# Optimization experiments

Measured on AMD Instinct MI355X. Metric: run time of the kernel, lower is better.

Reference implementation:

```python
import jax, jax.numpy as jnp
import numpy as np

NB = 5  # frequency bands


def _ln(x, g, b, eps=1e-5):
    m = jnp.mean(x, axis=-1, keepdims=True)
    v = jnp.var(x, axis=-1, keepdims=True)
    return (x - m) / jnp.sqrt(v + eps) * g + b


def _graph_adj(x, adj_w, sw1, sb1, sw2, sb2, pos_factor, pos_enc):
    # x: [B, D, N] -> degree-normalized adjacency [B, N, N]
    d = x.shape[1]
    xt = jnp.swapaxes(x, 1, 2)  # [B, N, D]
    # concat-MLP first layer split: cat(xi, xj) @ W1 == xi @ W1[:d] + xj @ W1[d:]
    a = xt @ sw1[:d]
    bpart = xt @ sw1[d:]
    h = jax.nn.elu(a[:, :, None, :] + bpart[:, None, :, :] + sb1)  # [B, N, N, H]
    dyn = jax.nn.sigmoid(jnp.squeeze(h @ sw2, -1) + sb2)  # [B, N, N]
    static = jax.nn.softmax(adj_w, axis=-1)
    pos = jax.nn.softmax(pos_enc, axis=-1)
    comb = jax.nn.softmax(static + dyn + pos_factor * pos, axis=-1)
    deg = jnp.sum(comb, axis=-1)
    dis = (deg + 1e-8) ** -0.5
    return dis[:, :, None] * comb * dis[:, None, :]


def _gcn(x, adj, w, b):
    # x: [B, D, N], adj: [B, N, N] -> [B, D_out, N]
    xt = jnp.swapaxes(x, 1, 2)
    out = jnp.einsum('bij,bjd->bid', adj, xt) @ w + b
    return jnp.swapaxes(out, 1, 2)


def _mha(x, qkv_w, qkv_b, ow, ob, nh=4):
    B, S, D = x.shape
    dh = D // nh
    q, k, v = jnp.split(x @ qkv_w + qkv_b, 3, axis=-1)
    q = q.reshape(B, S, nh, dh)
    k = k.reshape(B, S, nh, dh)
    v = v.reshape(B, S, nh, dh)
    att = jax.nn.softmax(jnp.einsum('bihd,bjhd->bhij', q, k) / float(np.sqrt(dh)), axis=-1)
    o = jnp.einsum('bhij,bjhd->bihd', att, v).reshape(B, S, D)
    return o @ ow + ob


def setup_inputs():
    key = jax.random.key(0)
    B, D, N = 16, 256, 64
    ks = iter(jax.random.split(key, 40))

    def rn(shape, s=0.05):
        return jax.random.normal(next(ks), shape, dtype=jnp.float32) * s

    eyeN = jnp.eye(N, dtype=jnp.float32)
    return dict(
        feature=jax.random.normal(next(ks), (B, NB * D, 1, N), dtype=jnp.float32),
        l_adj_w=jnp.tile(eyeN[None], (NB, 1, 1)),
        l_sim_w1=rn((NB, 2 * D, D)), l_sim_b1=jnp.zeros((NB, D), jnp.float32),
        l_sim_w2=rn((NB, D, 1)), l_sim_b2=jnp.zeros((NB, 1), jnp.float32),
        l_pos_factor=jnp.full((NB,), 0.5, jnp.float32),
        l_pos_enc=jnp.tile(eyeN[None], (NB, 1, 1)),
        l_gcn_w=rn((NB, D, D)), l_gcn_b=jnp.zeros((NB, D), jnp.float32),
        g_adj_w=jnp.eye(NB, dtype=jnp.float32),
        g_sim_w1=rn((2 * D, D)), g_sim_b1=jnp.zeros((D,), jnp.float32),
        g_sim_w2=rn((D, 1)), g_sim_b2=jnp.zeros((1,), jnp.float32),
        g_pos_factor=jnp.float32(0.5),
        g_pos_enc=jnp.eye(NB, dtype=jnp.float32),
        g_gcn_w=rn((D, D)), g_gcn_b=jnp.zeros((D,), jnp.float32),
        qkv_w=rn((D, 3 * D)), qkv_b=jnp.zeros((3 * D,), jnp.float32),
        attn_ow=rn((D, D)), attn_ob=jnp.zeros((D,), jnp.float32),
        ln1_g=jnp.ones((D,), jnp.float32), ln1_b=jnp.zeros((D,), jnp.float32),
        ln2_g=jnp.ones((D,), jnp.float32), ln2_b=jnp.zeros((D,), jnp.float32),
        mlp_w1=rn((D, 4 * D)), mlp_b1=jnp.zeros((4 * D,), jnp.float32),
        mlp_w2=rn((4 * D, D)), mlp_b2=jnp.zeros((D,), jnp.float32),
        imp_w=rn((NB, N, 1)), imp_b=jnp.zeros((NB, 1), jnp.float32),
    )


def reference(feature, l_adj_w, l_sim_w1, l_sim_b1, l_sim_w2, l_sim_b2,
              l_pos_factor, l_pos_enc, l_gcn_w, l_gcn_b,
              g_adj_w, g_sim_w1, g_sim_b1, g_sim_w2, g_sim_b2,
              g_pos_factor, g_pos_enc, g_gcn_w, g_gcn_b,
              qkv_w, qkv_b, attn_ow, attn_ob,
              ln1_g, ln1_b, ln2_g, ln2_b,
              mlp_w1, mlp_b1, mlp_w2, mlp_b2,
              imp_w, imp_b):
    B = feature.shape[0]
    D = l_gcn_w.shape[-1]
    N = feature.shape[-1]
    # [B, 5*D, 1, N] -> [5, B, D, N] band-major
    x5 = jnp.moveaxis(feature.reshape(B, NB, D, N), 1, 0)
    # per-band local graphs + GCNs (vmapped over the 5 bands)
    local_adj = jax.vmap(_graph_adj)(x5, l_adj_w, l_sim_w1, l_sim_b1,
                                     l_sim_w2, l_sim_b2, l_pos_factor, l_pos_enc)
    local_out = jax.vmap(_gcn)(x5, local_adj, l_gcn_w, l_gcn_b)  # [5, B, D, N]
    scale_nodes = jnp.moveaxis(jnp.mean(local_out, axis=-1), 0, 1)  # [B, 5, D]
    # cross-band attention block (pre: MHA + residual + LN, then MLP + residual + LN)
    attn = _mha(scale_nodes, qkv_w, qkv_b, attn_ow, attn_ob)
    h1 = _ln(scale_nodes + attn, ln1_g, ln1_b)
    mlp = jax.nn.gelu(h1 @ mlp_w1 + mlp_b1, approximate=False) @ mlp_w2 + mlp_b2
    se = _ln(h1 + mlp, ln2_g, ln2_b)  # [B, 5, D]
    # global scale graph over the 5 band nodes
    xg = jnp.swapaxes(se, 1, 2)  # [B, D, 5]
    g_adj = _graph_adj(xg, g_adj_w, g_sim_w1, g_sim_b1, g_sim_w2, g_sim_b2,
                       g_pos_factor, g_pos_enc)
    g_out = jnp.swapaxes(_gcn(xg, g_adj, g_gcn_w, g_gcn_b), 1, 2)  # [B, 5, D]
    # modulate each local band feature by its global scale vector
    enh = local_out * jnp.moveaxis(g_out, 1, 0)[..., None]  # [5, B, D, N]
    # per-band importance projection over channels: [5, B, D, 1]
    out5 = jnp.einsum('kbdn,kno->kbdo', enh, imp_w) + imp_b[:, None, None, :]
    output = jnp.moveaxis(out5, 0, 1).reshape(B, NB * D, 1, 1)
    return output, g_adj, jnp.moveaxis(local_out, 0, 1)
```

## Files before the change

kernel.cpp:

```cpp
#include <hip/hip_runtime.h>
#include <hip/hip_bf16.h>

#define NBANDS 5
#define BATCH  16
#define DIM    256
#define NNODE  64
#define SEQ    5
#define NHEAD  4
#define DHEAD  64

typedef __hip_bfloat16 bf16;
typedef unsigned short ushort_t;
typedef __attribute__((ext_vector_type(8))) short short8;
typedef __attribute__((ext_vector_type(4))) float float4v;

__device__ __forceinline__ float bu2f(ushort_t u){
    bf16 h = *reinterpret_cast<bf16*>(&u);
    return __bfloat162float(h);
}
__device__ __forceinline__ ushort_t f2bu(float x){
    bf16 h = __float2bfloat16(x);
    return *reinterpret_cast<ushort_t*>(&h);
}

__global__ void __launch_bounds__(256) k_head(
    const float* __restrict__ l_adj_w, const float* __restrict__ l_pos_enc,
    const float* __restrict__ l_pf,
    const float* __restrict__ g_adj_w, const float* __restrict__ g_pos_enc,
    const float* __restrict__ g_pf,
    float* __restrict__ sbase, float* __restrict__ gbase,
    const float* __restrict__ w1, const float* __restrict__ gw,
    ushort_t* __restrict__ w1bt, ushort_t* __restrict__ gwbt,
    const float* __restrict__ feat,
    ushort_t* __restrict__ xtb, ushort_t* __restrict__ xtT)
{
    int blk = blockIdx.x;
    int tid = threadIdx.x;
    __shared__ ushort_t tile[64][65];

    if (blk < 80) {
        int r = blk*4 + (tid>>6);
        int k = r >> 6, i = r & 63;
        int t = tid & 63;
        float aw = l_adj_w[(k*NNODE + i)*NNODE + t];
        float pe = l_pos_enc[(k*NNODE + i)*NNODE + t];
        float m1 = aw, m2 = pe;
        for (int o=32;o>0;o>>=1){ m1 = fmaxf(m1, __shfl_xor(m1,o,64)); m2 = fmaxf(m2, __shfl_xor(m2,o,64)); }
        float e1 = __expf(aw-m1), e2 = __expf(pe-m2);
        float s1=e1, s2=e2;
        for (int o=32;o>0;o>>=1){ s1 += __shfl_xor(s1,o,64); s2 += __shfl_xor(s2,o,64); }
        float pf = l_pf[k];
        sbase[(k*NNODE+i)*NNODE + t] = e1/s1 + pf*(e2/s2);
    } else if (blk == 80) {
        if (tid < NBANDS) {
            int i = tid;
            float r1[NBANDS], r2[NBANDS];
            float m1=-1e30f, m2=-1e30f;
            for (int j=0;j<NBANDS;j++){
                r1[j]=g_adj_w[i*NBANDS+j]; r2[j]=g_pos_enc[i*NBANDS+j];
                m1=fmaxf(m1,r1[j]); m2=fmaxf(m2,r2[j]);
            }
            float s1=0.f,s2=0.f;
            for (int j=0;j<NBANDS;j++){ r1[j]=__expf(r1[j]-m1); r2[j]=__expf(r2[j]-m2); s1+=r1[j]; s2+=r2[j]; }
            float pf = g_pf[0];
            for (int j=0;j<NBANDS;j++) gbase[i*NBANDS+j] = r1[j]/s1 + pf*(r2[j]/s2);
        }
    } else if (blk < 321) {
        int idx = blk - 81;
        int inst = idx >> 4;
        int t = idx & 15;
        int r0 = (t>>2)*64, c0 = (t&3)*64;
        const float* src; ushort_t* dst;
        if (inst < 10){
            int k = inst>>1, half = inst&1;
            src = w1  + ((size_t)k*512 + half*256)*256;
            dst = w1bt+ ((size_t)k*512 + half*256)*256;
        } else {
            int k = inst-10;
            src = gw  + (size_t)k*65536;
            dst = gwbt+ (size_t)k*65536;
        }
        int jj = tid & 63, i4 = tid >> 6;
        for (int p=0;p<16;p++){
            int i = p*4 + i4;
            tile[i][jj] = f2bu(src[(size_t)(r0+i)*256 + c0 + jj]);
        }
        __syncthreads();
        for (int p=0;p<16;p++){
            int i = p*4 + i4;
            dst[(size_t)(c0+i)*256 + r0 + jj] = tile[jj][i];
        }
    } else {
        int idx = blk - 321;
        int k = idx >> 6;
        int b = (idx >> 2) & 15;
        int dt = idx & 3;
        const float* src = feat + ((size_t)b*NBANDS*DIM + (size_t)k*DIM)*NNODE;
        ushort_t* dst = xtb + (size_t)(k*BATCH+b)*NNODE*DIM;
        ushort_t* dstT = xtT + (size_t)(k*BATCH+b)*DIM*NNODE;
        for (int u=0; u<16; ++u){
            int i = dt*4096 + u*256 + tid;
            dstT[i] = f2bu(src[i]);
        }
        for (int r=0;r<16;r++){
            int dp = r*4 + (tid>>6);
            int n  = tid & 63;
            tile[dp][n] = f2bu(src[(size_t)(dt*64+dp)*NNODE + n]);
        }
        __syncthreads();
        for (int r=0;r<16;r++){
            int n  = r*4 + (tid>>6);
            int dp = tid & 63;
            dst[(size_t)n*DIM + dt*64 + dp] = tile[dp][n];
        }
    }
}

__global__ void __launch_bounds__(256) k_ab_mfma(const ushort_t* __restrict__ xtb,
                        const ushort_t* __restrict__ w1bt, const float* __restrict__ b1,
                        ushort_t* __restrict__ aab, ushort_t* __restrict__ bbb)
{
    int blk = blockIdx.x;
    int kband = blk / (BATCH*8);
    int b = (blk/8) % BATCH;
    int nblk = blk & 7;
    int tid = threadIdx.x;
    int wave = tid>>6, lane = tid&63;
    int c16 = lane & 15, quad = lane >> 4;
    int m0 = wave*16;
    size_t rowbase = (size_t)(kband*BATCH+b)*NNODE;
    const ushort_t* Aptr = xtb + (rowbase + m0 + c16)*DIM + quad*8;
    const ushort_t* Bbase = w1bt + (size_t)kband*512*DIM;
    int ncol0 = nblk*64;
    const ushort_t* Bptr0 = Bbase + (size_t)(ncol0 +  0 + c16)*DIM + quad*8;
    const ushort_t* Bptr1 = Bbase + (size_t)(ncol0 + 16 + c16)*DIM + quad*8;
    const ushort_t* Bptr2 = Bbase + (size_t)(ncol0 + 32 + c16)*DIM + quad*8;
    const ushort_t* Bptr3 = Bbase + (size_t)(ncol0 + 48 + c16)*DIM + quad*8;
    float4v acc0 = {0.f,0.f,0.f,0.f}, acc1 = acc0, acc2 = acc0, acc3 = acc0;
    #pragma unroll
    for (int ks=0; ks<8; ++ks){
        short8 a  = *reinterpret_cast<const short8*>(Aptr  + ks*32);
        short8 b0 = *reinterpret_cast<const short8*>(Bptr0 + ks*32);
        short8 b1v= *reinterpret_cast<const short8*>(Bptr1 + ks*32);
        short8 b2 = *reinterpret_cast<const short8*>(Bptr2 + ks*32);
        short8 b3 = *reinterpret_cast<const short8*>(Bptr3 + ks*32);
        acc0 = __builtin_amdgcn_mfma_f32_16x16x32_bf16(a, b0, acc0, 0,0,0);
        acc1 = __builtin_amdgcn_mfma_f32_16x16x32_bf16(a, b1v, acc1, 0,0,0);
        acc2 = __builtin_amdgcn_mfma_f32_16x16x32_bf16(a, b2, acc2, 0,0,0);
        acc3 = __builtin_amdgcn_mfma_f32_16x16x32_bf16(a, b3, acc3, 0,0,0);
    }
    int half = nblk >> 2;
    int cbase = (nblk & 3)*64;
    ushort_t* dst = half ? bbb : aab;
    float4v accs[4] = {acc0, acc1, acc2, acc3};
    #pragma unroll
    for (int nt=0; nt<4; ++nt){
        int cg = cbase + nt*16 + c16;
        float bias = half ? 0.f : b1[kband*DIM + cg];
        #pragma unroll
        for (int r=0;r<4;r++){
            int m = m0 + quad*4 + r;
            dst[(rowbase + m)*DIM + cg] = f2bu(accs[nt][r] + bias);
        }
    }
}

__global__ void __launch_bounds__(256) k_dyn_comb(const ushort_t* __restrict__ aab,
                           const ushort_t* __restrict__ bbb,
                           const float* __restrict__ w2, const float* __restrict__ b2arr,
                           const float* __restrict__ sbase,
                           ushort_t* __restrict__ combb)
{
    int blk = blockIdx.x;
    int k = blk / (BATCH*16);
    int b = (blk / 16) % BATCH;
    int i0 = (blk % 16) * 4;
    int kb = k*BATCH + b;
    __shared__ ushort_t bs[64][260];
    __shared__ float arows[4][DIM];
    __shared__ float w2s[DIM];
    int tid = threadIdx.x;
    int wave = tid >> 6, lane = tid & 63;
    const ushort_t* bsrc = bbb + (size_t)kb*NNODE*DIM;
    for (int u=0; u<16; ++u){
        int idx = u*1024 + tid*4;
        int row = idx >> 8, col = idx & 255;
        *reinterpret_cast<ushort4*>(&bs[row][col]) =
            *reinterpret_cast<const ushort4*>(&bsrc[(size_t)row*DIM + col]);
    }
    for (int r=0;r<4;r++) arows[r][tid] = bu2f(aab[((size_t)kb*NNODE + i0 + r)*DIM + tid]);
    w2s[tid] = w2[k*DIM + tid];
    __syncthreads();

    int i = i0 + wave;
    float acc = 0.f;
    #pragma unroll 4
    for (int dd=0; dd<64; ++dd){
        ushort4 bv = *reinterpret_cast<const ushort4*>(&bs[lane][dd*4]);
        float4 av = *reinterpret_cast<const float4*>(&arows[wave][dd*4]);
        float4 wv = *reinterpret_cast<const float4*>(&w2s[dd*4]);
        float v0 = av.x + bu2f(bv.x);
        float v1 = av.y + bu2f(bv.y);
        float v2 = av.z + bu2f(bv.z);
        float v3 = av.w + bu2f(bv.w);
        float e0 = (v0>0.f)? v0 : (__expf(v0)-1.f);
        float e1 = (v1>0.f)? v1 : (__expf(v1)-1.f);
        float e2 = (v2>0.f)? v2 : (__expf(v2)-1.f);
        float e3 = (v3>0.f)? v3 : (__expf(v3)-1.f);
        acc += e0*wv.x + e1*wv.y + e2*wv.z + e3*wv.w;
    }
    float sb2 = b2arr[k];
    float sg = 1.f/(1.f + __expf(-(acc + sb2)));
    float val = sbase[(k*NNODE + i)*NNODE + lane] + sg;
    float m = val;
    for (int o=32;o>0;o>>=1) m = fmaxf(m, __shfl_xor(m,o,64));
    float e = __expf(val - m);
    float s = e;
    for (int o=32;o>0;o>>=1) s += __shfl_xor(s,o,64);
    combb[((size_t)kb*NNODE + i)*NNODE + lane] = f2bu(e/s);
}

__global__ void __launch_bounds__(256) k_y_mfma(const ushort_t* __restrict__ combb,
                       const ushort_t* __restrict__ xtT,
                       ushort_t* __restrict__ yb)
{
    int blk = blockIdx.x;
    int kband = blk / (BATCH*4);
    int b = (blk/4) % BATCH;
    int nblk = blk & 3;
    int tid = threadIdx.x;
    int wave = tid>>6, lane = tid&63;
    int c16 = lane & 15, quad = lane >> 4;
    int m0 = wave*16;
    int kb = kband*BATCH + b;
    const ushort_t* Aptr = combb + ((size_t)kb*NNODE + m0 + c16)*NNODE + quad*8;
    const ushort_t* Bbase = xtT + (size_t)kb*DIM*NNODE;
    int ncol0 = nblk*64;
    const ushort_t* Bptr0 = Bbase + (size_t)(ncol0 +  0 + c16)*NNODE + quad*8;
    const ushort_t* Bptr1 = Bbase + (size_t)(ncol0 + 16 + c16)*NNODE + quad*8;
    const ushort_t* Bptr2 = Bbase + (size_t)(ncol0 + 32 + c16)*NNODE + quad*8;
    const ushort_t* Bptr3 = Bbase + (size_t)(ncol0 + 48 + c16)*NNODE + quad*8;
    float4v acc0 = {0.f,0.f,0.f,0.f}, acc1 = acc0, acc2 = acc0, acc3 = acc0;
    #pragma unroll
    for (int ks=0; ks<2; ++ks){
        short8 a  = *reinterpret_cast<const short8*>(Aptr  + ks*32);
        short8 b0 = *reinterpret_cast<const short8*>(Bptr0 + ks*32);
        short8 b1v= *reinterpret_cast<const short8*>(Bptr1 + ks*32);
        short8 b2 = *reinterpret_cast<const short8*>(Bptr2 + ks*32);
        short8 b3 = *reinterpret_cast<const short8*>(Bptr3 + ks*32);
        acc0 = __builtin_amdgcn_mfma_f32_16x16x32_bf16(a, b0, acc0, 0,0,0);
        acc1 = __builtin_amdgcn_mfma_f32_16x16x32_bf16(a, b1v, acc1, 0,0,0);
        acc2 = __builtin_amdgcn_mfma_f32_16x16x32_bf16(a, b2, acc2, 0,0,0);
        acc3 = __builtin_amdgcn_mfma_f32_16x16x32_bf16(a, b3, acc3, 0,0,0);
    }
    size_t rowbase = (size_t)kb*NNODE;
    float4v accs[4] = {acc0, acc1, acc2, acc3};
    #pragma unroll
    for (int nt=0; nt<4; ++nt){
        int cg = ncol0 + nt*16 + c16;
        #pragma unroll
        for (int r=0;r<4;r++){
            int m = m0 + quad*4 + r;
            yb[(rowbase + m)*DIM + cg] = f2bu(accs[nt][r]);
        }
    }
}

__global__ void __launch_bounds__(256) k_gcn_mfma(const ushort_t* __restrict__ yb,
                         const ushort_t* __restrict__ gwbt, const float* __restrict__ gb,
                         const float* __restrict__ imp_w,
                         float* __restrict__ out_local,
                         float* __restrict__ scalew, float* __restrict__ impw)
{
    int blk = blockIdx.x;
    int kband = blk / (BATCH*4);
    int b = (blk/4) % BATCH;
    int nblk = blk & 3;
    int tid = threadIdx.x;
    int wave = tid>>6, lane = tid&63;
    int c16 = lane & 15, quad = lane >> 4;
    int m0 = wave*16;
    int kb = kband*BATCH + b;
    __shared__ float iw_s[NNODE];
    __shared__ float sred[4][64];
    __shared__ float ired[4][64];
    if (tid < NNODE) iw_s[tid] = imp_w[kband*NNODE + tid];
    const ushort_t* Aptr = yb + ((size_t)kb*NNODE + m0 + c16)*DIM + quad*8;
    const ushort_t* Bbase = gwbt + (size_t)kband*DIM*DIM;
    int ncol0 = nblk*64;
    const ushort_t* Bptr0 = Bbase + (size_t)(ncol0 +  0 + c16)*DIM + quad*8;
    const ushort_t* Bptr1 = Bbase + (size_t)(ncol0 + 16 + c16)*DIM + quad*8;
    const ushort_t* Bptr2 = Bbase + (size_t)(ncol0 + 32 + c16)*DIM + quad*8;
    const ushort_t* Bptr3 = Bbase + (size_t)(ncol0 + 48 + c16)*DIM + quad*8;
    float4v acc0 = {0.f,0.f,0.f,0.f}, acc1 = acc0, acc2 = acc0, acc3 = acc0;
    #pragma unroll
    for (int ks=0; ks<8; ++ks){
        short8 a  = *reinterpret_cast<const short8*>(Aptr  + ks*32);
        short8 b0 = *reinterpret_cast<const short8*>(Bptr0 + ks*32);
        short8 b1v= *reinterpret_cast<const short8*>(Bptr1 + ks*32);
        short8 b2 = *reinterpret_cast<const short8*>(Bptr2 + ks*32);
        short8 b3 = *reinterpret_cast<const short8*>(Bptr3 + ks*32);
        acc0 = __builtin_amdgcn_mfma_f32_16x16x32_bf16(a, b0, acc0, 0,0,0);
        acc1 = __builtin_amdgcn_mfma_f32_16x16x32_bf16(a, b1v, acc1, 0,0,0);
        acc2 = __builtin_amdgcn_mfma_f32_16x16x32_bf16(a, b2, acc2, 0,0,0);
        acc3 = __builtin_amdgcn_mfma_f32_16x16x32_bf16(a, b3, acc3, 0,0,0);
    }
    __syncthreads();
    float4v accs[4] = {acc0, acc1, acc2, acc3};
    #pragma unroll
    for (int nt=0; nt<4; ++nt){
        int cg = ncol0 + nt*16 + c16;
        float bias = gb[kband*DIM + cg];
        float v0 = accs[nt][0]+bias, v1 = accs[nt][1]+bias, v2 = accs[nt][2]+bias, v3 = accs[nt][3]+bias;
        float4 v = make_float4(v0, v1, v2, v3);
        float* dst = out_local + ((size_t)(b*NBANDS + kband)*DIM + cg)*NNODE + m0 + quad*4;
        *reinterpret_cast<float4*>(dst) = v;
        int nb = m0 + quad*4;
        float s  = v0 + v1 + v2 + v3;
        float di = v0*iw_s[nb] + v1*iw_s[nb+1] + v2*iw_s[nb+2] + v3*iw_s[nb+3];
        s  += __shfl_xor(s, 16, 64);  s  += __shfl_xor(s, 32, 64);
        di += __shfl_xor(di, 16, 64); di += __shfl_xor(di, 32, 64);
        if (quad == 0){
            sred[wave][nt*16 + c16] = s;
            ired[wave][nt*16 + c16] = di;
        }
    }
    __syncthreads();
    if (tid < 64){
        float s  = sred[0][tid] + sred[1][tid] + sred[2][tid] + sred[3][tid];
        float di = ired[0][tid] + ired[1][tid] + ired[2][tid] + ired[3][tid];
        size_t o = ((size_t)b*SEQ + kband)*DIM + ncol0 + tid;
        scalew[o] = s * (1.f/64.f);
        impw[o]   = di;
    }
}

template<int COLS, int SLICES>
__global__ void __launch_bounds__(256) k_gemv(const float* __restrict__ x, const float* __restrict__ w,
                       const float* __restrict__ bias, float* __restrict__ out,
                       int K, int N, int act)
{
    int chunks = N / COLS;
    int row = blockIdx.x / chunks;
    int n0 = (blockIdx.x % chunks) * COLS;
    int c = threadIdx.x % COLS, s = threadIdx.x / COLS;
    __shared__ float xs[1024];
    __shared__ float part[SLICES][COLS];
    for (int i = threadIdx.x; i < K; i += 256) xs[i] = x[(size_t)row*K + i];
    __syncthreads();
    int klen = K / SLICES;
    const float* wp = w + (size_t)(s*klen)*N + n0 + c;
    const float* xp = xs + s*klen;
    float acc = 0.f;
    #pragma unroll 8
    for (int i = 0; i < klen; ++i) acc += xp[i] * wp[(size_t)i*N];
    part[s][c] = acc;
    __syncthreads();
    if (s == 0){
        float v = bias[n0+c];
        #pragma unroll
        for (int q=0;q<SLICES;q++) v += part[q][c];
        if (act) v = 0.5f*v*(1.f + erff(v*0.70710678118654752f));
        out[(size_t)row*N + n0 + c] = v;
    }
}

__global__ void __launch_bounds__(256) k_projattn(const float* __restrict__ qkvw,
                        const float* __restrict__ ow, const float* __restrict__ ob,
                        float* __restrict__ projw)
{
    int row = blockIdx.x / 4;
    int n0 = (blockIdx.x % 4) * 64;
    int b = row / SEQ, i = row % SEQ;
    int tid = threadIdx.x;
    int h = tid >> 6, l = tid & 63;
    __shared__ float xs[DIM];
    __shared__ float part[4][64];
    const float* base = qkvw + (size_t)b*SEQ*3*DIM;
    float qv = base[(size_t)i*3*DIM + h*DHEAD + l];
    float pj[SEQ];
    #pragma unroll
    for (int j=0;j<SEQ;j++){
        float p = qv * base[(size_t)j*3*DIM + DIM + h*DHEAD + l];
        for (int o=32;o>0;o>>=1) p += __shfl_xor(p,o,64);
        pj[j] = p * 0.125f;
    }
    float m = pj[0];
    #pragma unroll
    for (int j=1;j<SEQ;j++) m = fmaxf(m, pj[j]);
    float ssum = 0.f;
    #pragma unroll
    for (int j=0;j<SEQ;j++){ pj[j] = __expf(pj[j]-m); ssum += pj[j]; }
    float inv = 1.f/ssum;
    float o = 0.f;
    #pragma unroll
    for (int j=0;j<SEQ;j++) o += pj[j]*inv * base[(size_t)j*3*DIM + 2*DIM + h*DHEAD + l];
    xs[tid] = o;
    __syncthreads();
    int c = tid & 63, s = tid >> 6;
    const float* wp = ow + (size_t)(s*64)*DIM + n0 + c;
    const float* xp = xs + s*64;
    float acc = 0.f;
    #pragma unroll 8
    for (int k=0;k<64;++k) acc += xp[k] * wp[(size_t)k*DIM];
    part[s][c] = acc;
    __syncthreads();
    if (s == 0){
        projw[(size_t)row*DIM + n0 + c] = ob[n0+c] + part[0][c]+part[1][c]+part[2][c]+part[3][c];
    }
}

__device__ __forceinline__ float block_ln(float v, int tid, float* red, float g, float bln)
{
    float s = v;
    for (int o=32;o>0;o>>=1) s += __shfl_xor(s,o,64);
    int wave = tid>>6, lane = tid&63;
    if (lane==0) red[wave] = s;
    __syncthreads();
    float mean = (red[0]+red[1]+red[2]+red[3]) * (1.f/DIM);
    float c = v - mean;
    float q = c*c;
    for (int o=32;o>0;o>>=1) q += __shfl_xor(q,o,64);
    __syncthreads();
    if (lane==0) red[wave] = q;
    __syncthreads();
    float var = (red[0]+red[1]+red[2]+red[3]) * (1.f/DIM);
    return c * rsqrtf(var + 1e-5f) * g + bln;
}

__global__ void __launch_bounds__(256) k_mlp1_ln(const float* __restrict__ projw,
                         const float* __restrict__ scalew,
                         const float* __restrict__ ln1_g, const float* __restrict__ ln1_b,
                         const float* __restrict__ w1, const float* __restrict__ b1,
                         float* __restrict__ h1w, float* __restrict__ mhw)
{
    int row = blockIdx.x / 16;
    int n0 = (blockIdx.x % 16) * 64;
    int tid = threadIdx.x;
    __shared__ float xs[DIM];
    __shared__ float red[4];
    __shared__ float part[4][64];
    float v = projw[(size_t)row*DIM + tid] + scalew[(size_t)row*DIM + tid];
    float h = block_ln(v, tid, red, ln1_g[tid], ln1_b[tid]);
    xs[tid] = h;
    if ((blockIdx.x % 16) == 0) h1w[(size_t)row*DIM + tid] = h;
    __syncthreads();
    int c = tid & 63, s = tid >> 6;
    const float* wp = w1 + (size_t)(s*64)*1024 + n0 + c;
    const float* xp = xs + s*64;
    float acc = 0.f;
    #pragma unroll 8
    for (int i=0;i<64;++i) acc += xp[i] * wp[(size_t)i*1024];
    part[s][c] = acc;
    __syncthreads();
    if (s == 0){
        float o = b1[n0+c] + part[0][c] + part[1][c] + part[2][c] + part[3][c];
        o = 0.5f*o*(1.f + erff(o*0.70710678118654752f));
        mhw[(size_t)row*1024 + n0 + c] = o;
    }
}

__global__ void __launch_bounds__(256) k_gab_ln(const float* __restrict__ m2w,
                        const float* __restrict__ h1w,
                        const float* __restrict__ ln2_g, const float* __restrict__ ln2_b,
                        const float* __restrict__ gw1, const float* __restrict__ gb1,
                        float* __restrict__ sew, float* __restrict__ gaw, float* __restrict__ gbw)
{
    int row = blockIdx.x / 4;
    int n0 = (blockIdx.x % 4) * 64;
    int tid = threadIdx.x;
    __shared__ float xs[DIM];
    __shared__ float red[4];
    __shared__ float partA[4][64];
    __shared__ float partB[4][64];
    float v = m2w[(size_t)row*DIM + tid] + h1w[(size_t)row*DIM + tid];
    float h = block_ln(v, tid, red, ln2_g[tid], ln2_b[tid]);
    xs[tid] = h;
    if ((blockIdx.x % 4) == 0) sew[(size_t)row*DIM + tid] = h;
    __syncthreads();
    int c = tid & 63, s = tid >> 6;
    const float* wpA = gw1 + (size_t)(s*64)*DIM + n0 + c;
    const float* wpB = wpA + (size_t)DIM*DIM;
    const float* xp = xs + s*64;
    float aA = 0.f, aB = 0.f;
    #pragma unroll 8
    for (int i=0;i<64;++i){
        float xv = xp[i];
        aA += xv * wpA[(size_t)i*DIM];
        aB += xv * wpB[(size_t)i*DIM];
    }
    partA[s][c] = aA;
    partB[s][c] = aB;
    __syncthreads();
    if (s == 0){
        gaw[(size_t)row*DIM + n0 + c] = gb1[n0+c] + partA[0][c]+partA[1][c]+partA[2][c]+partA[3][c];
        gbw[(size_t)row*DIM + n0 + c] = partB[0][c]+partB[1][c]+partB[2][c]+partB[3][c];
    }
}

__global__ void __launch_bounds__(256) k_goutfin(const float* __restrict__ gaw,
                        const float* __restrict__ gbw,
                        const float* __restrict__ gw2, const float* __restrict__ gb2,
                        const float* __restrict__ gbase,
                        const float* __restrict__ sew,
                        const float* __restrict__ ggw, const float* __restrict__ ggb,
                        const float* __restrict__ impw, const float* __restrict__ imp_b,
                        float* __restrict__ out0, float* __restrict__ out_gadj)
{
    int row = blockIdx.x / 4;
    int n0 = (blockIdx.x % 4) * 64;
    int b = row / SEQ, i = row % SEQ;
    int tid = threadIdx.x;
    int wave = tid >> 6, lane = tid & 63;
    __shared__ float dyn_s[SEQ];
    __shared__ float xs[DIM];
    __shared__ float part[4][64];
    for (int j = wave; j < SEQ; j += 4){
        const float* gar = gaw + (size_t)row*DIM;
        const float* gbr = gbw + ((size_t)b*SEQ + j)*DIM;
        float acc = 0.f;
        #pragma unroll
        for (int m=0;m<4;m++){
            int dd = lane + m*64;
            float v = gar[dd] + gbr[dd];
            float e = (v>0.f) ? v : (__expf(v)-1.f);
            acc += e * gw2[dd];
        }
        for (int o=32;o>0;o>>=1) acc += __shfl_xor(acc,o,64);
        if (lane==0) dyn_s[j] = acc;
    }
    __syncthreads();
    float gc[SEQ];
    {
        float sb2 = gb2[0];
        float m = -1e30f;
        #pragma unroll
        for (int j=0;j<SEQ;j++){
            float sg = 1.f/(1.f+__expf(-(dyn_s[j]+sb2)));
            gc[j] = gbase[i*SEQ+j] + sg;
            m = fmaxf(m, gc[j]);
        }
        float ssum=0.f;
        #pragma unroll
        for (int j=0;j<SEQ;j++){ gc[j]=__expf(gc[j]-m); ssum+=gc[j]; }
        float inv = 1.f/ssum;
        #pragma unroll
        for (int j=0;j<SEQ;j++) gc[j] *= inv;
    }
    if (n0 == 0 && tid < SEQ) out_gadj[((size_t)b*SEQ+i)*SEQ + tid] = gc[tid];
    float t = 0.f;
    #pragma unroll
    for (int j=0;j<SEQ;j++) t += gc[j]*sew[((size_t)b*SEQ + j)*DIM + tid];
    xs[tid] = t;
    __syncthreads();
    int c = tid & 63, s = tid >> 6;
    const float* wp = ggw + (size_t)(s*64)*DIM + n0 + c;
    const float* xp = xs + s*64;
    float acc = 0.f;
    #pragma unroll 8
    for (int k=0;k<64;++k) acc += xp[k] * wp[(size_t)k*DIM];
    part[s][c] = acc;
    __syncthreads();
    if (s == 0){
        float g = ggb[n0+c] + part[0][c]+part[1][c]+part[2][c]+part[3][c];
        size_t o = (size_t)row*DIM + n0 + c;
        out0[o] = g * impw[o] + imp_b[i];
    }
}

extern "C" void kernel_launch(void* const* d_in, const int* in_sizes, int n_in,
                              void* d_out, int out_size, void* d_ws, size_t ws_size,
                              hipStream_t stream)
{
    const float* feature      = (const float*)d_in[0];
    const float* l_adj_w      = (const float*)d_in[1];
    const float* l_sim_w1     = (const float*)d_in[2];
    const float* l_sim_b1     = (const float*)d_in[3];
    const float* l_sim_w2     = (const float*)d_in[4];
    const float* l_sim_b2     = (const float*)d_in[5];
    const float* l_pos_factor = (const float*)d_in[6];
    const float* l_pos_enc    = (const float*)d_in[7];
    const float* l_gcn_w      = (const float*)d_in[8];
    const float* l_gcn_b      = (const float*)d_in[9];
    const float* g_adj_w      = (const float*)d_in[10];
    const float* g_sim_w1     = (const float*)d_in[11];
    const float* g_sim_b1     = (const float*)d_in[12];
    const float* g_sim_w2     = (const float*)d_in[13];
    const float* g_sim_b2     = (const float*)d_in[14];
    const float* g_pos_factor = (const float*)d_in[15];
    const float* g_pos_enc    = (const float*)d_in[16];
    const float* g_gcn_w      = (const float*)d_in[17];
    const float* g_gcn_b      = (const float*)d_in[18];
    const float* qkv_w        = (const float*)d_in[19];
    const float* qkv_b        = (const float*)d_in[20];
    const float* attn_ow      = (const float*)d_in[21];
    const float* attn_ob      = (const float*)d_in[22];
    const float* ln1_g        = (const float*)d_in[23];
    const float* ln1_b        = (const float*)d_in[24];
    const float* ln2_g        = (const float*)d_in[25];
    const float* ln2_b        = (const float*)d_in[26];
    const float* mlp_w1       = (const float*)d_in[27];
    const float* mlp_b1       = (const float*)d_in[28];
    const float* mlp_w2       = (const float*)d_in[29];
    const float* mlp_b2       = (const float*)d_in[30];
    const float* imp_w        = (const float*)d_in[31];
    const float* imp_b        = (const float*)d_in[32];

    float* out0      = (float*)d_out;
    float* out_gadj  = out0 + (size_t)BATCH*NBANDS*DIM;
    float* out_local = out_gadj + (size_t)BATCH*NBANDS*NBANDS;

    const size_t BIG = (size_t)NBANDS*BATCH*NNODE*DIM;
    ushort_t* xtb   = (ushort_t*)d_ws;
    ushort_t* aab   = xtb + BIG;
    ushort_t* bbb   = aab + BIG;
    ushort_t* xtT   = bbb + BIG;
    ushort_t* yb    = aab;
    ushort_t* w1bt  = xtT + BIG;
    ushort_t* gwbt  = w1bt + (size_t)NBANDS*512*DIM;
    ushort_t* combb = gwbt + (size_t)NBANDS*DIM*DIM;
    float* fp = (float*)(combb + (size_t)NBANDS*BATCH*NNODE*NNODE);
    float* sbase  = fp; fp += NBANDS*NNODE*NNODE;
    float* gbase  = fp; fp += 32;
    float* scalew = fp; fp += BATCH*SEQ*DIM;
    float* impw   = fp; fp += BATCH*SEQ*DIM;
    float* qkvw   = fp; fp += BATCH*SEQ*3*DIM;
    float* projw  = fp; fp += BATCH*SEQ*DIM;
    float* h1w    = fp; fp += BATCH*SEQ*DIM;
    float* mhw    = fp; fp += BATCH*SEQ*4*DIM;
    float* m2w    = fp; fp += BATCH*SEQ*DIM;
    float* sew    = fp; fp += BATCH*SEQ*DIM;
    float* gaw    = fp; fp += BATCH*SEQ*DIM;
    float* gbw    = fp; fp += BATCH*SEQ*DIM;

    const int ROWS = BATCH*SEQ;

    k_head<<<641, 256, 0, stream>>>(l_adj_w, l_pos_enc, l_pos_factor,
                                    g_adj_w, g_pos_enc, g_pos_factor,
                                    sbase, gbase,
                                    l_sim_w1, l_gcn_w, w1bt, gwbt,
                                    feature, xtb, xtT);
    k_ab_mfma<<<NBANDS*BATCH*8, 256, 0, stream>>>(xtb, w1bt, l_sim_b1, aab, bbb);
    k_dyn_comb<<<NBANDS*BATCH*16, 256, 0, stream>>>(aab, bbb, l_sim_w2, l_sim_b2, sbase, combb);
    k_y_mfma<<<NBANDS*BATCH*4, 256, 0, stream>>>(combb, xtT, yb);
    k_gcn_mfma<<<NBANDS*BATCH*4, 256, 0, stream>>>(yb, gwbt, l_gcn_b, imp_w,
                                                   out_local, scalew, impw);
    k_gemv<64,4><<<ROWS*12, 256, 0, stream>>>(scalew, qkv_w, qkv_b, qkvw, 256, 768, 0);
    k_projattn<<<ROWS*4, 256, 0, stream>>>(qkvw, attn_ow, attn_ob, projw);
    k_mlp1_ln<<<ROWS*16, 256, 0, stream>>>(projw, scalew, ln1_g, ln1_b, mlp_w1, mlp_b1, h1w, mhw);
    k_gemv<32,8><<<ROWS*8, 256, 0, stream>>>(mhw, mlp_w2, mlp_b2, m2w, 1024, 256, 0);
    k_gab_ln<<<ROWS*4, 256, 0, stream>>>(m2w, h1w, ln2_g, ln2_b, g_sim_w1, g_sim_b1, sew, gaw, gbw);
    k_goutfin<<<ROWS*4, 256, 0, stream>>>(gaw, gbw, g_sim_w2, g_sim_b2, gbase,
                                          sew, g_gcn_w, g_gcn_b, impw, imp_b,
                                          out0, out_gadj);
}
```

Measured before the change: 218.3 us.

## Fuse GCN tail with QKV projection and collapse attention/MLP chain into fewer kernels

Restructures the post-GCN pipeline so that one block per (band,batch) computes the full GCN output tile, reduces the node means, and immediately runs the QKV projection. Attention projection, residual and LN1 are then fused into one kernel, and both MLP layers, LN2 and the global-graph first layer into another. This removes several launches and intermediate buffers. In exchange it cuts parallelism sharply: 80 blocks instead of 320 or more per stage, and each thread walks long serial dot-product loops over the weights. Those long loops may become latency-bound on a GPU with many CUs.

```diff
diff --git a/kernel.cpp b/kernel.cpp
--- a/kernel.cpp
+++ b/kernel.cpp
@@ -266,148 +266,92 @@
     }
 }
 
-__global__ void __launch_bounds__(256) k_gcn_mfma(const ushort_t* __restrict__ yb,
-                         const ushort_t* __restrict__ gwbt, const float* __restrict__ gb,
-                         const float* __restrict__ imp_w,
-                         float* __restrict__ out_local,
-                         float* __restrict__ scalew, float* __restrict__ impw)
+__global__ void __launch_bounds__(256) k_gcn_qkv(const ushort_t* __restrict__ yb,
+                        const ushort_t* __restrict__ gwbt, const float* __restrict__ gb,
+                        const float* __restrict__ imp_w,
+                        const float* __restrict__ qkv_w, const float* __restrict__ qkv_b,
+                        float* __restrict__ out_local,
+                        float* __restrict__ scalew, float* __restrict__ impw,
+                        float* __restrict__ qkvw)
 {
     int blk = blockIdx.x;
-    int kband = blk / (BATCH*4);
-    int b = (blk/4) % BATCH;
-    int nblk = blk & 3;
+    int kband = blk / BATCH;
+    int b = blk % BATCH;
+    int kb = kband*BATCH + b;
     int tid = threadIdx.x;
     int wave = tid>>6, lane = tid&63;
     int c16 = lane & 15, quad = lane >> 4;
-    int m0 = wave*16;
-    int kb = kband*BATCH + b;
+    int ncol0 = wave*64;
     __shared__ float iw_s[NNODE];
-    __shared__ float sred[4][64];
-    __shared__ float ired[4][64];
+    __shared__ float s_lds[DIM];
     if (tid < NNODE) iw_s[tid] = imp_w[kband*NNODE + tid];
-    const ushort_t* Aptr = yb + ((size_t)kb*NNODE + m0 + c16)*DIM + quad*8;
+    __syncthreads();
+
     const ushort_t* Bbase = gwbt + (size_t)kband*DIM*DIM;
-    int ncol0 = nblk*64;
     const ushort_t* Bptr0 = Bbase + (size_t)(ncol0 +  0 + c16)*DIM + quad*8;
     const ushort_t* Bptr1 = Bbase + (size_t)(ncol0 + 16 + c16)*DIM + quad*8;
     const ushort_t* Bptr2 = Bbase + (size_t)(ncol0 + 32 + c16)*DIM + quad*8;
     const ushort_t* Bptr3 = Bbase + (size_t)(ncol0 + 48 + c16)*DIM + quad*8;
-    float4v acc0 = {0.f,0.f,0.f,0.f}, acc1 = acc0, acc2 = acc0, acc3 = acc0;
-    #pragma unroll
-    for (int ks=0; ks<8; ++ks){
-        short8 a  = *reinterpret_cast<const short8*>(Aptr  + ks*32);
-        short8 b0 = *reinterpret_cast<const short8*>(Bptr0 + ks*32);
-        short8 b1v= *reinterpret_cast<const short8*>(Bptr1 + ks*32);
-        short8 b2 = *reinterpret_cast<const short8*>(Bptr2 + ks*32);
-        short8 b3 = *reinterpret_cast<const short8*>(Bptr3 + ks*32);
-        acc0 = __builtin_amdgcn_mfma_f32_16x16x32_bf16(a, b0, acc0, 0,0,0);
-        acc1 = __builtin_amdgcn_mfma_f32_16x16x32_bf16(a, b1v, acc1, 0,0,0);
-        acc2 = __builtin_amdgcn_mfma_f32_16x16x32_bf16(a, b2, acc2, 0,0,0);
-        acc3 = __builtin_amdgcn_mfma_f32_16x16x32_bf16(a, b3, acc3, 0,0,0);
-    }
-    __syncthreads();
-    float4v accs[4] = {acc0, acc1, acc2, acc3};
+
+    float sacc[4] = {0.f,0.f,0.f,0.f};
+    float dacc[4] = {0.f,0.f,0.f,0.f};
+
+    for (int rt=0; rt<4; ++rt){
+        const ushort_t* Aptr = yb + ((size_t)kb*NNODE + rt*16 + c16)*DIM + quad*8;
+        float4v acc0 = {0.f,0.f,0.f,0.f}, acc1 = acc0, acc2 = acc0, acc3 = acc0;
+        #pragma unroll
+        for (int ks=0; ks<8; ++ks){
+            short8 a  = *reinterpret_cast<const short8*>(Aptr  + ks*32);
+            short8 b0 = *reinterpret_cast<const short8*>(Bptr0 + ks*32);
+            short8 b1v= *reinterpret_cast<const short8*>(Bptr1 + ks*32);
+            short8 b2 = *reinterpret_cast<const short8*>(Bptr2 + ks*32);
+            short8 b3 = *reinterpret_cast<const short8*>(Bptr3 + ks*32);
+            acc0 = __builtin_amdgcn_mfma_f32_16x16x32_bf16(a, b0, acc0, 0,0,0);
+            acc1 = __builtin_amdgcn_mfma_f32_16x16x32_bf16(a, b1v, acc1, 0,0,0);
+            acc2 = __builtin_amdgcn_mfma_f32_16x16x32_bf16(a, b2, acc2, 0,0,0);
+            acc3 = __builtin_amdgcn_mfma_f32_16x16x32_bf16(a, b3, acc3, 0,0,0);
+        }
+        float4v accs[4] = {acc0, acc1, acc2, acc3};
+        #pragma unroll
+        for (int nt=0; nt<4; ++nt){
+            int cg = ncol0 + nt*16 + c16;
+            float bias = gb[kband*DIM + cg];
+            float v0 = accs[nt][0]+bias, v1 = accs[nt][1]+bias,
+                  v2 = accs[nt][2]+bias, v3 = accs[nt][3]+bias;
+            float4 v = make_float4(v0, v1, v2, v3);
+            float* dst = out_local + ((size_t)(b*NBANDS + kband)*DIM + cg)*NNODE + rt*16 + quad*4;
+            *reinterpret_cast<float4*>(dst) = v;
+            int nb = rt*16 + quad*4;
+            sacc[nt] += v0 + v1 + v2 + v3;
+            dacc[nt] += v0*iw_s[nb] + v1*iw_s[nb+1] + v2*iw_s[nb+2] + v3*iw_s[nb+3];
+        }
+    }
+    size_t row = (size_t)b*SEQ + kband;
     #pragma unroll
     for (int nt=0; nt<4; ++nt){
-        int cg = ncol0 + nt*16 + c16;
-        float bias = gb[kband*DIM + cg];
-        float v0 = accs[nt][0]+bias, v1 = accs[nt][1]+bias, v2 = accs[nt][2]+bias, v3 = accs[nt][3]+bias;
-        float4 v = make_float4(v0, v1, v2, v3);
-        float* dst = out_local + ((size_t)(b*NBANDS + kband)*DIM + cg)*NNODE + m0 + quad*4;
-        *reinterpret_cast<float4*>(dst) = v;
-        int nb = m0 + quad*4;
-        float s  = v0 + v1 + v2 + v3;
-        float di = v0*iw_s[nb] + v1*iw_s[nb+1] + v2*iw_s[nb+2] + v3*iw_s[nb+3];
-        s  += __shfl_xor(s, 16, 64);  s  += __shfl_xor(s, 32, 64);
-        di += __shfl_xor(di, 16, 64); di += __shfl_xor(di, 32, 64);
+        float s = sacc[nt], d = dacc[nt];
+        s += __shfl_xor(s, 16, 64);  s += __shfl_xor(s, 32, 64);
+        d += __shfl_xor(d, 16, 64);  d += __shfl_xor(d, 32, 64);
         if (quad == 0){
-            sred[wave][nt*16 + c16] = s;
-            ired[wave][nt*16 + c16] = di;
-        }
-    }
-    __syncthreads();
-    if (tid < 64){
-        float s  = sred[0][tid] + sred[1][tid] + sred[2][tid] + sred[3][tid];
-        float di = ired[0][tid] + ired[1][tid] + ired[2][tid] + ired[3][tid];
-        size_t o = ((size_t)b*SEQ + kband)*DIM + ncol0 + tid;
-        scalew[o] = s * (1.f/64.f);
-        impw[o]   = di;
-    }
-}
-
-template<int COLS, int SLICES>
-__global__ void __launch_bounds__(256) k_gemv(const float* __restrict__ x, const float* __restrict__ w,
-                       const float* __restrict__ bias, float* __restrict__ out,
-                       int K, int N, int act)
-{
-    int chunks = N / COLS;
-    int row = blockIdx.x / chunks;
-    int n0 = (blockIdx.x % chunks) * COLS;
-    int c = threadIdx.x % COLS, s = threadIdx.x / COLS;
-    __shared__ float xs[1024];
-    __shared__ float part[SLICES][COLS];
-    for (int i = threadIdx.x; i < K; i += 256) xs[i] = x[(size_t)row*K + i];
-    __syncthreads();
-    int klen = K / SLICES;
-    const float* wp = w + (size_t)(s*klen)*N + n0 + c;
-    const float* xp = xs + s*klen;
-    float acc = 0.f;
-    #pragma unroll 8
-    for (int i = 0; i < klen; ++i) acc += xp[i] * wp[(size_t)i*N];
-    part[s][c] = acc;
-    __syncthreads();
-    if (s == 0){
-        float v = bias[n0+c];
-        #pragma unroll
-        for (int q=0;q<SLICES;q++) v += part[q][c];
-        if (act) v = 0.5f*v*(1.f + erff(v*0.70710678118654752f));
-        out[(size_t)row*N + n0 + c] = v;
-    }
-}
-
-__global__ void __launch_bounds__(256) k_projattn(const float* __restrict__ qkvw,
-                        const float* __restrict__ ow, const float* __restrict__ ob,
-                        float* __restrict__ projw)
-{
-    int row = blockIdx.x / 4;
-    int n0 = (blockIdx.x % 4) * 64;
-    int b = row / SEQ, i = row % SEQ;
-    int tid = threadIdx.x;
-    int h = tid >> 6, l = tid & 63;
-    __shared__ float xs[DIM];
-    __shared__ float part[4][64];
-    const float* base = qkvw + (size_t)b*SEQ*3*DIM;
-    float qv = base[(size_t)i*3*DIM + h*DHEAD + l];
-    float pj[SEQ];
-    #pragma unroll
-    for (int j=0;j<SEQ;j++){
-        float p = qv * base[(size_t)j*3*DIM + DIM + h*DHEAD + l];
-        for (int o=32;o>0;o>>=1) p += __shfl_xor(p,o,64);
-        pj[j] = p * 0.125f;
-    }
-    float m = pj[0];
-    #pragma unroll
-    for (int j=1;j<SEQ;j++) m = fmaxf(m, pj[j]);
-    float ssum = 0.f;
-    #pragma unroll
-    for (int j=0;j<SEQ;j++){ pj[j] = __expf(pj[j]-m); ssum += pj[j]; }
-    float inv = 1.f/ssum;
-    float o = 0.f;
-    #pragma unroll
-    for (int j=0;j<SEQ;j++) o += pj[j]*inv * base[(size_t)j*3*DIM + 2*DIM + h*DHEAD + l];
-    xs[tid] = o;
-    __syncthreads();
-    int c = tid & 63, s = tid >> 6;
-    const float* wp = ow + (size_t)(s*64)*DIM + n0 + c;
-    const float* xp = xs + s*64;
-    float acc = 0.f;
-    #pragma unroll 8
-    for (int k=0;k<64;++k) acc += xp[k] * wp[(size_t)k*DIM];
-    part[s][c] = acc;
-    __syncthreads();
-    if (s == 0){
-        projw[(size_t)row*DIM + n0 + c] = ob[n0+c] + part[0][c]+part[1][c]+part[2][c]+part[3][c];
-    }
+            int cg = ncol0 + nt*16 + c16;
+            float sv = s * (1.f/64.f);
+            scalew[row*DIM + cg] = sv;
+            impw[row*DIM + cg]   = d;
+            s_lds[cg] = sv;
+        }
+    }
+    __syncthreads();
+    float a0 = 0.f, a1 = 0.f, a2 = 0.f;
+    for (int kk=0; kk<DIM; ++kk){
+        float x = s_lds[kk];
+        const float* wp = qkv_w + (size_t)kk*768;
+        a0 += x * wp[tid];
+        a1 += x * wp[256 + tid];
+        a2 += x * wp[512 + tid];
+    }
+    qkvw[row*768 + tid]       = a0 + qkv_b[tid];
+    qkvw[row*768 + 256 + tid] = a1 + qkv_b[256 + tid];
+    qkvw[row*768 + 512 + tid] = a2 + qkv_b[512 + tid];
 }
 
 __device__ __forceinline__ float block_ln(float v, int tid, float* red, float g, float bln)
@@ -428,74 +372,90 @@
     return c * rsqrtf(var + 1e-5f) * g + bln;
 }
 
-__global__ void __launch_bounds__(256) k_mlp1_ln(const float* __restrict__ projw,
-                         const float* __restrict__ scalew,
-                         const float* __restrict__ ln1_g, const float* __restrict__ ln1_b,
-                         const float* __restrict__ w1, const float* __restrict__ b1,
-                         float* __restrict__ h1w, float* __restrict__ mhw)
-{
-    int row = blockIdx.x / 16;
-    int n0 = (blockIdx.x % 16) * 64;
-    int tid = threadIdx.x;
+__global__ void __launch_bounds__(256) k_projattn_ln1(const float* __restrict__ qkvw,
+                        const float* __restrict__ ow, const float* __restrict__ ob,
+                        const float* __restrict__ scalew,
+                        const float* __restrict__ ln1_g, const float* __restrict__ ln1_b,
+                        float* __restrict__ h1w)
+{
+    int row = blockIdx.x;
+    int b = row / SEQ, i = row % SEQ;
+    int tid = threadIdx.x;
+    int h = tid >> 6, l = tid & 63;
     __shared__ float xs[DIM];
     __shared__ float red[4];
-    __shared__ float part[4][64];
-    float v = projw[(size_t)row*DIM + tid] + scalew[(size_t)row*DIM + tid];
-    float h = block_ln(v, tid, red, ln1_g[tid], ln1_b[tid]);
-    xs[tid] = h;
-    if ((blockIdx.x % 16) == 0) h1w[(size_t)row*DIM + tid] = h;
-    __syncthreads();
-    int c = tid & 63, s = tid >> 6;
-    const float* wp = w1 + (size_t)(s*64)*1024 + n0 + c;
-    const float* xp = xs + s*64;
+    const float* base = qkvw + (size_t)b*SEQ*3*DIM;
+    float qv = base[(size_t)i*3*DIM + h*DHEAD + l];
+    float pj[SEQ];
+    #pragma unroll
+    for (int j=0;j<SEQ;j++){
+        float pr = qv * base[(size_t)j*3*DIM + DIM + h*DHEAD + l];
+        for (int o=32;o>0;o>>=1) pr += __shfl_xor(pr,o,64);
+        pj[j] = pr * 0.125f;
+    }
+    float m = pj[0];
+    #pragma unroll
+    for (int j=1;j<SEQ;j++) m = fmaxf(m, pj[j]);
+    float ssum = 0.f;
+    #pragma unroll
+    for (int j=0;j<SEQ;j++){ pj[j] = __expf(pj[j]-m); ssum += pj[j]; }
+    float inv = 1.f/ssum;
+    float o = 0.f;
+    #pragma unroll
+    for (int j=0;j<SEQ;j++) o += pj[j]*inv * base[(size_t)j*3*DIM + 2*DIM + h*DHEAD + l];
+    xs[tid] = o;
+    __syncthreads();
     float acc = 0.f;
     #pragma unroll 8
-    for (int i=0;i<64;++i) acc += xp[i] * wp[(size_t)i*1024];
-    part[s][c] = acc;
-    __syncthreads();
-    if (s == 0){
-        float o = b1[n0+c] + part[0][c] + part[1][c] + part[2][c] + part[3][c];
-        o = 0.5f*o*(1.f + erff(o*0.70710678118654752f));
-        mhw[(size_t)row*1024 + n0 + c] = o;
-    }
-}
-
-__global__ void __launch_bounds__(256) k_gab_ln(const float* __restrict__ m2w,
-                        const float* __restrict__ h1w,
+    for (int dp=0; dp<DIM; ++dp) acc += xs[dp] * ow[(size_t)dp*DIM + tid];
+    float v = acc + ob[tid] + scalew[(size_t)row*DIM + tid];
+    float h1 = block_ln(v, tid, red, ln1_g[tid], ln1_b[tid]);
+    h1w[(size_t)row*DIM + tid] = h1;
+}
+
+__global__ void __launch_bounds__(256) k_mlp_gab(const float* __restrict__ h1w,
+                        const float* __restrict__ w1, const float* __restrict__ b1,
+                        const float* __restrict__ w2, const float* __restrict__ b2v,
                         const float* __restrict__ ln2_g, const float* __restrict__ ln2_b,
                         const float* __restrict__ gw1, const float* __restrict__ gb1,
                         float* __restrict__ sew, float* __restrict__ gaw, float* __restrict__ gbw)
 {
-    int row = blockIdx.x / 4;
-    int n0 = (blockIdx.x % 4) * 64;
+    int row = blockIdx.x;
     int tid = threadIdx.x;
     __shared__ float xs[DIM];
+    __shared__ float hid[4*DIM];
     __shared__ float red[4];
-    __shared__ float partA[4][64];
-    __shared__ float partB[4][64];
-    float v = m2w[(size_t)row*DIM + tid] + h1w[(size_t)row*DIM + tid];
-    float h = block_ln(v, tid, red, ln2_g[tid], ln2_b[tid]);
-    xs[tid] = h;
-    if ((blockIdx.x % 4) == 0) sew[(size_t)row*DIM + tid] = h;
-    __syncthreads();
-    int c = tid & 63, s = tid >> 6;
-    const float* wpA = gw1 + (size_t)(s*64)*DIM + n0 + c;
-    const float* wpB = wpA + (size_t)DIM*DIM;
-    const float* xp = xs + s*64;
+    float h1 = h1w[(size_t)row*DIM + tid];
+    xs[tid] = h1;
+    __syncthreads();
+    #pragma unroll
+    for (int c=0;c<4;c++){
+        int col = c*256 + tid;
+        float acc = 0.f;
+        #pragma unroll 8
+        for (int dp=0; dp<DIM; ++dp) acc += xs[dp] * w1[(size_t)dp*1024 + col];
+        acc += b1[col];
+        hid[col] = 0.5f*acc*(1.f + erff(acc*0.70710678118654752f));
+    }
+    __syncthreads();
+    float acc2 = 0.f;
+    #pragma unroll 8
+    for (int dp=0; dp<1024; ++dp) acc2 += hid[dp] * w2[(size_t)dp*DIM + tid];
+    float v = acc2 + b2v[tid] + h1;
+    float se = block_ln(v, tid, red, ln2_g[tid], ln2_b[tid]);
+    sew[(size_t)row*DIM + tid] = se;
+    __syncthreads();
+    xs[tid] = se;
+    __syncthreads();
     float aA = 0.f, aB = 0.f;
     #pragma unroll 8
-    for (int i=0;i<64;++i){
-        float xv = xp[i];
-        aA += xv * wpA[(size_t)i*DIM];
-        aB += xv * wpB[(size_t)i*DIM];
-    }
-    partA[s][c] = aA;
-    partB[s][c] = aB;
-    __syncthreads();
-    if (s == 0){
-        gaw[(size_t)row*DIM + n0 + c] = gb1[n0+c] + partA[0][c]+partA[1][c]+partA[2][c]+partA[3][c];
-        gbw[(size_t)row*DIM + n0 + c] = partB[0][c]+partB[1][c]+partB[2][c]+partB[3][c];
-    }
+    for (int dp=0; dp<DIM; ++dp){
+        float xv = xs[dp];
+        aA += xv * gw1[(size_t)dp*DIM + tid];
+        aB += xv * gw1[(size_t)(DIM+dp)*DIM + tid];
+    }
+    gaw[(size_t)row*DIM + tid] = aA + gb1[tid];
+    gbw[(size_t)row*DIM + tid] = aB;
 }
 
 __global__ void __launch_bounds__(256) k_goutfin(const float* __restrict__ gaw,
@@ -625,15 +585,10 @@
     float* scalew = fp; fp += BATCH*SEQ*DIM;
     float* impw   = fp; fp += BATCH*SEQ*DIM;
     float* qkvw   = fp; fp += BATCH*SEQ*3*DIM;
-    float* projw  = fp; fp += BATCH*SEQ*DIM;
     float* h1w    = fp; fp += BATCH*SEQ*DIM;
-    float* mhw    = fp; fp += BATCH*SEQ*4*DIM;
-    float* m2w    = fp; fp += BATCH*SEQ*DIM;
     float* sew    = fp; fp += BATCH*SEQ*DIM;
     float* gaw    = fp; fp += BATCH*SEQ*DIM;
     float* gbw    = fp; fp += BATCH*SEQ*DIM;
-
-    const int ROWS = BATCH*SEQ;
 
     k_head<<<641, 256, 0, stream>>>(l_adj_w, l_pos_enc, l_pos_factor,
                                     g_adj_w, g_pos_enc, g_pos_factor,
@@ -643,14 +598,14 @@
     k_ab_mfma<<<NBANDS*BATCH*8, 256, 0, stream>>>(xtb, w1bt, l_sim_b1, aab, bbb);
     k_dyn_comb<<<NBANDS*BATCH*16, 256, 0, stream>>>(aab, bbb, l_sim_w2, l_sim_b2, sbase, combb);
     k_y_mfma<<<NBANDS*BATCH*4, 256, 0, stream>>>(combb, xtT, yb);
-    k_gcn_mfma<<<NBANDS*BATCH*4, 256, 0, stream>>>(yb, gwbt, l_gcn_b, imp_w,
-                                                   out_local, scalew, impw);
-    k_gemv<64,4><<<ROWS*12, 256, 0, stream>>>(scalew, qkv_w, qkv_b, qkvw, 256, 768, 0);
-    k_projattn<<<ROWS*4, 256, 0, stream>>>(qkvw, attn_ow, attn_ob, projw);
-    k_mlp1_ln<<<ROWS*16, 256, 0, stream>>>(projw, scalew, ln1_g, ln1_b, mlp_w1, mlp_b1, h1w, mhw);
-    k_gemv<32,8><<<ROWS*8, 256, 0, stream>>>(mhw, mlp_w2, mlp_b2, m2w, 1024, 256, 0);
-    k_gab_ln<<<ROWS*4, 256, 0, stream>>>(m2w, h1w, ln2_g, ln2_b, g_sim_w1, g_sim_b1, sew, gaw, gbw);
-    k_goutfin<<<ROWS*4, 256, 0, stream>>>(gaw, gbw, g_sim_w2, g_sim_b2, gbase,
-                                          sew, g_gcn_w, g_gcn_b, impw, imp_b,
-                                          out0, out_gadj);
-}
+    k_gcn_qkv<<<NBANDS*BATCH, 256, 0, stream>>>(yb, gwbt, l_gcn_b, imp_w, qkv_w, qkv_b,
+                                                out_local, scalew, impw, qkvw);
+    k_projattn_ln1<<<BATCH*SEQ, 256, 0, stream>>>(qkvw, attn_ow, attn_ob, scalew,
+                                                  ln1_g, ln1_b, h1w);
+    k_mlp_gab<<<BATCH*SEQ, 256, 0, stream>>>(h1w, mlp_w1, mlp_b1, mlp_w2, mlp_b2,
+                                             ln2_g, ln2_b, g_sim_w1, g_sim_b1,
+                                             sew, gaw, gbw);
+    k_goutfin<<<BATCH*SEQ*4, 256, 0, stream>>>(gaw, gbw, g_sim_w2, g_sim_b2, gbase,
+                                               sew, g_gcn_w, g_gcn_b, impw, imp_b,
+                                               out0, out_gadj);
+}
```

New measurement: 321.1 us. +47.1%, slower.
